# Kernel tuning notes

Hardware: AMD Instinct MI355X
Metric: run time of the kernel (lower is better)

Reference implementation:

```python
import jax, jax.numpy as jnp
import numpy as np

K_NN = 16  # number of nearest neighbors (module init arg k)


def setup_inputs() -> dict:
    key = jax.random.key(0)
    k1, k2 = jax.random.split(key)
    xyz = jax.random.normal(k1, (8, 16384, 3), dtype=jnp.float32)
    centers = jax.random.normal(k2, (8, 1024, 3), dtype=jnp.float32)
    return {"xyz": xyz, "centers": centers}


def reference(xyz, centers):
    # avoiding the (B, N, K, 3) broadcast intermediate of the original while
    # computing the same torch.norm(xyz - centers, dim=-1) math.
    x_sq = jnp.sum(xyz * xyz, axis=-1)          # (B, N)
    c_sq = jnp.sum(centers * centers, axis=-1)  # (B, K)
    cross = jnp.einsum('bnd,bkd->bnk', xyz, centers)  # (B, N, K)
    d2 = x_sq[:, :, None] + c_sq[None if False else slice(None), None, :] - 2.0 * cross
    dist = jnp.sqrt(jnp.maximum(d2, 0.0))       # (B, N, K)
    # torch.topk(dist, k, dim=1, largest=False, sorted=True):
    # smallest-k over the N (points) axis, per center.
    neg = -jnp.transpose(dist, (0, 2, 1))       # (B, K, N)
    _, idx = jax.lax.top_k(neg, K_NN)           # (B, K, k), ascending distance
    return jnp.transpose(idx, (0, 2, 1))        # (B, k, K) to match torch dim=1 topk
```

## Files before the change

kernel.cpp:

```cpp
#include <hip/hip_runtime.h>
#include <stdint.h>

#define BB    8
#define NN    16384
#define KK    1024
#define KNN   16
#define QTR   (NN / 4)
#define QGRP  (QTR / 4)
#define PGRP  256
#define HCAP  96

typedef unsigned long long u64;
typedef float f32x2 __attribute__((ext_vector_type(2)));

__device__ __forceinline__ f32x2 pk_fma(f32x2 a, f32x2 b, f32x2 c) {
    f32x2 d;
    asm("v_pk_fma_f32 %0, %1, %2, %3" : "=v"(d) : "v"(a), "v"(b), "v"(c));
    return d;
}
__device__ __forceinline__ f32x2 pk_mul(f32x2 a, f32x2 b) {
    f32x2 d;
    asm("v_pk_mul_f32 %0, %1, %2" : "=v"(d) : "v"(a), "v"(b));
    return d;
}
__device__ __forceinline__ f32x2 pk_add(f32x2 a, f32x2 b) {
    f32x2 d;
    asm("v_pk_add_f32 %0, %1, %2" : "=v"(d) : "v"(a), "v"(b));
    return d;
}

__device__ __forceinline__ u64 shfl_xor_u64(u64 v, int mask) {
    int lo = (int)(uint32_t)v;
    int hi = (int)(uint32_t)(v >> 32);
    lo = __shfl_xor(lo, mask, 64);
    hi = __shfl_xor(hi, mask, 64);
    return ((u64)(uint32_t)hi << 32) | (u64)(uint32_t)lo;
}

__device__ __forceinline__ u64 shfl_u64(u64 v, int src) {
    int lo = __shfl((int)(uint32_t)v, src, 64);
    int hi = __shfl((int)(uint32_t)(v >> 32), src, 64);
    return ((u64)(uint32_t)hi << 32) | (u64)(uint32_t)lo;
}

__device__ __forceinline__ u64 wave_min_u64(u64 v) {
#pragma unroll
    for (int off = 32; off > 0; off >>= 1) {
        u64 o = shfl_xor_u64(v, off);
        v = o < v ? o : v;
    }
    return v;
}

__device__ __forceinline__ void sort64_kv(u64& key, uint32_t& pay, int lane) {
#pragma unroll
    for (int k = 2; k <= 64; k <<= 1) {
#pragma unroll
        for (int j = k >> 1; j > 0; j >>= 1) {
            u64 okey = shfl_xor_u64(key, j);
            uint32_t opay = (uint32_t)__shfl_xor((int)pay, j, 64);
            bool tmin = ((lane & j) == 0) == ((lane & k) == 0);
            bool osm = okey < key;
            bool take = tmin ? osm : !osm;
            if (take) { key = okey; pay = opay; }
        }
    }
}

__device__ __forceinline__ void sort64_k(u64& key, int lane) {
#pragma unroll
    for (int k = 2; k <= 64; k <<= 1) {
#pragma unroll
        for (int j = k >> 1; j > 0; j >>= 1) {
            u64 okey = shfl_xor_u64(key, j);
            bool tmin = ((lane & j) == 0) == ((lane & k) == 0);
            bool osm = okey < key;
            bool take = tmin ? osm : !osm;
            if (take) key = okey;
        }
    }
}

__device__ __forceinline__ float point_d2(const float* xb, int i,
                                          float c0, float c1, float c2, float csq) {
#pragma clang fp contract(off)
    float x0 = xb[i * 3 + 0];
    float x1 = xb[i * 3 + 1];
    float x2 = xb[i * 3 + 2];
    float xsq = (x0 * x0 + x1 * x1) + x2 * x2;
    float cross = __fmaf_rn(x2, c2, __fmaf_rn(x1, c1, x0 * c0));
    float d2 = (xsq + csq) - 2.0f * cross;
    return d2 < 0.0f ? 0.0f : d2;
}

__device__ __attribute__((noinline)) int fallback_scan(const float* xb,
                                                       float c0, float c1, float c2,
                                                       float csq, int lane) {
    u64 list[KNN];
#pragma unroll
    for (int j = 0; j < KNN; ++j) list[j] = ~0ull;
    for (int i = lane; i < NN; i += 64) {
        float d2 = point_d2(xb, i, c0, c1, c2, csq);
        float dist = __fsqrt_rn(d2);
        u64 key = ((u64)__float_as_uint(dist) << 32) | (u64)(uint32_t)i;
        if (key < list[KNN - 1]) {
#pragma unroll
            for (int j = 0; j < KNN; ++j) {
                bool lt = key < list[j];
                u64 lo = lt ? key : list[j];
                u64 hi = lt ? list[j] : key;
                list[j] = lo;
                key = hi;
            }
        }
    }
    int res = 0;
    for (int it = 0; it < KNN; ++it) {
        u64 best = wave_min_u64(list[0]);
        if (it == lane) res = (int)(uint32_t)best;
        if (list[0] == best) {
#pragma unroll
            for (int j = 0; j < KNN - 1; ++j) list[j] = list[j + 1];
            list[KNN - 1] = ~0ull;
        }
    }
    return res;
}

__device__ __forceinline__ float sixteenth_smallest(float m, int lane) {
    uint32_t u = __float_as_uint(m);
    uint32_t s = (u & 0x80000000u) ? ~u : (u | 0x80000000u);
    u64 v = ((u64)s << 32) | (unsigned)lane;
#pragma unroll
    for (int k = 2; k <= 64; k <<= 1) {
#pragma unroll
        for (int j = k >> 1; j > 0; j >>= 1) {
            u64 o = shfl_xor_u64(v, j);
            bool up = (lane & k) == 0;
            bool takeMin = ((lane & j) == 0) == up;
            u64 mn = v < o ? v : o;
            u64 mx = v < o ? o : v;
            v = takeMin ? mn : mx;
        }
    }
    uint32_t sb = (uint32_t)__shfl((int)(uint32_t)(v >> 32), 15, 64);
    uint32_t ub = (sb & 0x80000000u) ? (sb ^ 0x80000000u) : ~sb;
    return __uint_as_float(ub);
}

__device__ __forceinline__ void load_pairs_aos(const float4* x4, int g,
                                               f32x2& xl, f32x2& xh,
                                               f32x2& yl, f32x2& yh,
                                               f32x2& zl, f32x2& zh,
                                               f32x2& sl, f32x2& sh) {
    float4 f0 = x4[g * 3 + 0];
    float4 f1 = x4[g * 3 + 1];
    float4 f2 = x4[g * 3 + 2];
    xl = f32x2{f0.x, f0.w};  yl = f32x2{f0.y, f1.x};  zl = f32x2{f0.z, f1.y};
    xh = f32x2{f1.z, f2.y};  yh = f32x2{f1.w, f2.z};  zh = f32x2{f2.x, f2.w};
    sl = pk_add(pk_add(pk_mul(xl, xl), pk_mul(yl, yl)), pk_mul(zl, zl));
    sh = pk_add(pk_add(pk_mul(xh, xh), pk_mul(yh, yh)), pk_mul(zh, zh));
}

__global__ __launch_bounds__(256, 8) void knn_kernel(const float* __restrict__ xyz,
                                                     const float* __restrict__ centers,
                                                     int* __restrict__ out) {
#pragma clang fp contract(off)
    const int q = (int)(threadIdx.x >> 6);
    const int lane = (int)(threadIdx.x & 63);
    const int cbase = (int)blockIdx.x * 4;
    const int b = cbase >> 10;

    __shared__ float    s_min[4][256];
    __shared__ float    s_T[4];
    __shared__ int      s_cnt[4][4];
    __shared__ uint32_t s_idx[4][4][HCAP];

    f32x2 nx[4], ny[4], nz[4];
#pragma unroll
    for (int c = 0; c < 4; ++c) {
        float a0 = -2.0f * centers[(cbase + c) * 3 + 0];
        float a1 = -2.0f * centers[(cbase + c) * 3 + 1];
        float a2 = -2.0f * centers[(cbase + c) * 3 + 2];
        nx[c] = f32x2{a0, a0};
        ny[c] = f32x2{a1, a1};
        nz[c] = f32x2{a2, a2};
    }

    const float* xb = xyz + (size_t)b * NN * 3;
    const float4* x4 = (const float4*)xb;
    const int gbase = q * QGRP;

    float m[4];
#pragma unroll
    for (int c = 0; c < 4; ++c) m[c] = __builtin_inff();
#pragma unroll 2
    for (int s = 0; s < PGRP / 64; ++s) {
        int g = gbase + s * 64 + lane;
        f32x2 xl, xh, yl, yh, zl, zh, sl, sh;
        load_pairs_aos(x4, g, xl, xh, yl, yh, zl, zh, sl, sh);
#pragma unroll
        for (int c = 0; c < 4; ++c) {
            f32x2 dl = pk_fma(xl, nx[c], pk_fma(yl, ny[c], pk_fma(zl, nz[c], sl)));
            f32x2 dh = pk_fma(xh, nx[c], pk_fma(yh, ny[c], pk_fma(zh, nz[c], sh)));
            m[c] = fminf(m[c], fminf(fminf(dl.x, dl.y), fminf(dh.x, dh.y)));
        }
    }
#pragma unroll
    for (int c = 0; c < 4; ++c) s_min[c][threadIdx.x] = m[c];
    if (threadIdx.x < 16) s_cnt[threadIdx.x >> 2][threadIdx.x & 3] = 0;
    __syncthreads();
    {
        float v = fminf(fminf(s_min[q][lane], s_min[q][64 + lane]),
                        fminf(s_min[q][128 + lane], s_min[q][192 + lane]));
        float t = sixteenth_smallest(v, lane);
        if (lane == 0) s_T[q] = t;
    }
    __syncthreads();
    float U[4];
#pragma unroll
    for (int c = 0; c < 4; ++c) {
        float T = s_T[c];
        U[c] = T + fabsf(T) * 1e-5f + 5e-4f;
    }

#pragma unroll 2
    for (int s = 0; s < QGRP / 64; ++s) {
        int g = gbase + s * 64 + lane;
        f32x2 xl, xh, yl, yh, zl, zh, sl, sh;
        load_pairs_aos(x4, g, xl, xh, yl, yh, zl, zh, sl, sh);
        int ibase = g * 4;
#pragma unroll
        for (int c = 0; c < 4; ++c) {
            f32x2 dl = pk_fma(xl, nx[c], pk_fma(yl, ny[c], pk_fma(zl, nz[c], sl)));
            f32x2 dh = pk_fma(xh, nx[c], pk_fma(yh, ny[c], pk_fma(zh, nz[c], sh)));
            if (dl.x <= U[c]) {
                int pos = atomicAdd(&s_cnt[c][q], 1);
                if (pos < HCAP) s_idx[c][q][pos] = (uint32_t)(ibase + 0);
            }
            if (dl.y <= U[c]) {
                int pos = atomicAdd(&s_cnt[c][q], 1);
                if (pos < HCAP) s_idx[c][q][pos] = (uint32_t)(ibase + 1);
            }
            if (dh.x <= U[c]) {
                int pos = atomicAdd(&s_cnt[c][q], 1);
                if (pos < HCAP) s_idx[c][q][pos] = (uint32_t)(ibase + 2);
            }
            if (dh.y <= U[c]) {
                int pos = atomicAdd(&s_cnt[c][q], 1);
                if (pos < HCAP) s_idx[c][q][pos] = (uint32_t)(ibase + 3);
            }
        }
    }
    __syncthreads();

    const int cc = cbase + q;
    const float c0 = centers[cc * 3 + 0];
    const float c1 = centers[cc * 3 + 1];
    const float c2 = centers[cc * 3 + 2];
    const float csq = (c0 * c0 + c1 * c1) + c2 * c2;
    const int k0 = s_cnt[q][0], k1 = s_cnt[q][1], k2 = s_cnt[q][2], k3 = s_cnt[q][3];
    const int p1o = k0, p2o = k0 + k1, p3o = k0 + k1 + k2;
    const int total = p3o + k3;
    const bool ok = (k0 <= HCAP) & (k1 <= HCAP) & (k2 <= HCAP) & (k3 <= HCAP) &
                    (total <= 4 * 64);

    uint32_t res;
    if (ok) {
        u64 l0 = ~0ull, l1 = ~0ull, l2 = ~0ull, l3 = ~0ull;
        for (int j = lane; j < total; j += 64) {
            int qq, off;
            if (j < p1o)      { qq = 0; off = j; }
            else if (j < p2o) { qq = 1; off = j - p1o; }
            else if (j < p3o) { qq = 2; off = j - p2o; }
            else              { qq = 3; off = j - p3o; }
            int idx = (int)s_idx[q][qq][off];
            float d2 = point_d2(xb, idx, c0, c1, c2, csq);
            u64 key = ((u64)__float_as_uint(__fsqrt_rn(d2)) << 32) | (u64)(uint32_t)idx;
            bool t;
            t = key < l0; { u64 lo = t ? key : l0, hi = t ? l0 : key; l0 = lo; key = hi; }
            t = key < l1; { u64 lo = t ? key : l1, hi = t ? l1 : key; l1 = lo; key = hi; }
            t = key < l2; { u64 lo = t ? key : l2, hi = t ? l2 : key; l2 = lo; key = hi; }
            t = key < l3; { u64 lo = t ? key : l3, hi = t ? l3 : key; l3 = lo; key = hi; }
        }
        u64 key = l0;
        uint32_t pay = (uint32_t)lane;
        sort64_kv(key, pay, lane);
        int pos = lane >> 2, elem = lane & 3;
        int sid = __shfl((int)pay, pos, 64);
        u64 g0 = shfl_u64(l0, sid);
        u64 g1 = shfl_u64(l1, sid);
        u64 g2 = shfl_u64(l2, sid);
        u64 g3 = shfl_u64(l3, sid);
        u64 gk = (elem == 0) ? g0 : (elem == 1) ? g1 : (elem == 2) ? g2 : g3;
        sort64_k(gk, lane);
        res = (uint32_t)gk;
    } else {
        res = (uint32_t)fallback_scan(xb, c0, c1, c2, csq, lane);
    }

    if (lane < KNN) {
        out[((size_t)b * KNN + lane) * KK + (cc & 1023)] = (int)res;
    }
}

extern "C" void kernel_launch(void* const* d_in, const int* in_sizes, int n_in,
                              void* d_out, int out_size, void* d_ws, size_t ws_size,
                              hipStream_t stream) {
    const float* xyz = (const float*)d_in[0];
    const float* centers = (const float*)d_in[1];
    int* out = (int*)d_out;
    (void)d_ws; (void)ws_size;

    const int nblocks = BB * KK / 4;
    hipLaunchKernelGGL(knn_kernel, dim3(nblocks), dim3(256), 0, stream,
                       xyz, centers, out);
}
```

Baseline: 98.89 us.

## Replace sample-threshold plus full rescan with group-min pruning and targeted rescan

The kernel no longer builds a threshold from a sampled subset of points and then rescans all points against it. A single full pass now records the minimum partial distance of each 16-point group in shared memory. The 16th smallest of those group minima gives a threshold, and only groups under the threshold are re-evaluated to collect candidates. This removes one full distance pass and most of the per-point atomics, at the cost of a larger shared-memory footprint (s_gmin is 16 KB per block), extra shuffles, and a second, irregular gather pass.

After: 95.79 us. -3.1%, faster.

```diff
diff --git a/kernel.cpp b/kernel.cpp
--- a/kernel.cpp
+++ b/kernel.cpp
@@ -7,8 +7,9 @@
 #define KNN   16
 #define QTR   (NN / 4)
 #define QGRP  (QTR / 4)
-#define PGRP  256
-#define HCAP  96
+#define NG16  (NN / 16)
+#define GCAP  48
+#define SCAP  192
 
 typedef unsigned long long u64;
 typedef float f32x2 __attribute__((ext_vector_type(2)));
@@ -171,10 +172,11 @@
     const int cbase = (int)blockIdx.x * 4;
     const int b = cbase >> 10;
 
-    __shared__ float    s_min[4][256];
-    __shared__ float    s_T[4];
-    __shared__ int      s_cnt[4][4];
-    __shared__ uint32_t s_idx[4][4][HCAP];
+    __shared__ float    s_gmin[4][NG16];
+    __shared__ uint32_t s_glist[4][GCAP];
+    __shared__ uint32_t s_idx[4][SCAP];
+    __shared__ int      s_gcnt[4];
+    __shared__ int      s_cnt[4];
 
     f32x2 nx[4], ny[4], nz[4];
 #pragma unroll
@@ -191,97 +193,98 @@
     const float4* x4 = (const float4*)xb;
     const int gbase = q * QGRP;
 
-    float m[4];
-#pragma unroll
-    for (int c = 0; c < 4; ++c) m[c] = __builtin_inff();
-#pragma unroll 2
-    for (int s = 0; s < PGRP / 64; ++s) {
-        int g = gbase + s * 64 + lane;
-        f32x2 xl, xh, yl, yh, zl, zh, sl, sh;
-        load_pairs_aos(x4, g, xl, xh, yl, yh, zl, zh, sl, sh);
-#pragma unroll
-        for (int c = 0; c < 4; ++c) {
-            f32x2 dl = pk_fma(xl, nx[c], pk_fma(yl, ny[c], pk_fma(zl, nz[c], sl)));
-            f32x2 dh = pk_fma(xh, nx[c], pk_fma(yh, ny[c], pk_fma(zh, nz[c], sh)));
-            m[c] = fminf(m[c], fminf(fminf(dl.x, dl.y), fminf(dh.x, dh.y)));
-        }
-    }
-#pragma unroll
-    for (int c = 0; c < 4; ++c) s_min[c][threadIdx.x] = m[c];
-    if (threadIdx.x < 16) s_cnt[threadIdx.x >> 2][threadIdx.x & 3] = 0;
-    __syncthreads();
-    {
-        float v = fminf(fminf(s_min[q][lane], s_min[q][64 + lane]),
-                        fminf(s_min[q][128 + lane], s_min[q][192 + lane]));
-        float t = sixteenth_smallest(v, lane);
-        if (lane == 0) s_T[q] = t;
-    }
-    __syncthreads();
-    float U[4];
-#pragma unroll
-    for (int c = 0; c < 4; ++c) {
-        float T = s_T[c];
-        U[c] = T + fabsf(T) * 1e-5f + 5e-4f;
-    }
+    if (threadIdx.x < 4) { s_gcnt[threadIdx.x] = 0; s_cnt[threadIdx.x] = 0; }
 
 #pragma unroll 2
     for (int s = 0; s < QGRP / 64; ++s) {
         int g = gbase + s * 64 + lane;
         f32x2 xl, xh, yl, yh, zl, zh, sl, sh;
         load_pairs_aos(x4, g, xl, xh, yl, yh, zl, zh, sl, sh);
-        int ibase = g * 4;
+        float gm[4];
 #pragma unroll
         for (int c = 0; c < 4; ++c) {
             f32x2 dl = pk_fma(xl, nx[c], pk_fma(yl, ny[c], pk_fma(zl, nz[c], sl)));
             f32x2 dh = pk_fma(xh, nx[c], pk_fma(yh, ny[c], pk_fma(zh, nz[c], sh)));
-            if (dl.x <= U[c]) {
-                int pos = atomicAdd(&s_cnt[c][q], 1);
-                if (pos < HCAP) s_idx[c][q][pos] = (uint32_t)(ibase + 0);
-            }
-            if (dl.y <= U[c]) {
-                int pos = atomicAdd(&s_cnt[c][q], 1);
-                if (pos < HCAP) s_idx[c][q][pos] = (uint32_t)(ibase + 1);
-            }
-            if (dh.x <= U[c]) {
-                int pos = atomicAdd(&s_cnt[c][q], 1);
-                if (pos < HCAP) s_idx[c][q][pos] = (uint32_t)(ibase + 2);
-            }
-            if (dh.y <= U[c]) {
-                int pos = atomicAdd(&s_cnt[c][q], 1);
-                if (pos < HCAP) s_idx[c][q][pos] = (uint32_t)(ibase + 3);
-            }
+            float v = fminf(fminf(dl.x, dl.y), fminf(dh.x, dh.y));
+            v = fminf(v, __shfl_xor(v, 1, 64));
+            v = fminf(v, __shfl_xor(v, 2, 64));
+            gm[c] = v;
+        }
+        if ((lane & 3) == 0) {
+            int gi = g >> 2;
+#pragma unroll
+            for (int c = 0; c < 4; ++c) s_gmin[c][gi] = gm[c];
         }
     }
     __syncthreads();
+
+    float lm = __builtin_inff();
+#pragma unroll
+    for (int it = 0; it < NG16 / 64; ++it)
+        lm = fminf(lm, s_gmin[q][it * 64 + lane]);
+    float t = sixteenth_smallest(lm, lane);
+    const float Uq = t + fabsf(t) * 1e-5f + 5e-4f;
+
+#pragma unroll
+    for (int it = 0; it < NG16 / 64; ++it) {
+        int gi = it * 64 + lane;
+        if (s_gmin[q][gi] <= Uq) {
+            int pos = atomicAdd(&s_gcnt[q], 1);
+            if (pos < GCAP) s_glist[q][pos] = (uint32_t)gi;
+        }
+    }
+    __syncthreads();
+
+    const int ng = s_gcnt[q];
+    bool ok = (ng <= GCAP);
+
+    if (ok) {
+        for (int j = lane; j < ng * 4; j += 64) {
+            int lg = (int)s_glist[q][j >> 2] * 4 + (j & 3);
+            f32x2 xl, xh, yl, yh, zl, zh, sl, sh;
+            load_pairs_aos(x4, lg, xl, xh, yl, yh, zl, zh, sl, sh);
+            f32x2 dl = pk_fma(xl, nx[q], pk_fma(yl, ny[q], pk_fma(zl, nz[q], sl)));
+            f32x2 dh = pk_fma(xh, nx[q], pk_fma(yh, ny[q], pk_fma(zh, nz[q], sh)));
+            int ibase = lg * 4;
+            if (dl.x <= Uq) {
+                int pos = atomicAdd(&s_cnt[q], 1);
+                if (pos < SCAP) s_idx[q][pos] = (uint32_t)(ibase + 0);
+            }
+            if (dl.y <= Uq) {
+                int pos = atomicAdd(&s_cnt[q], 1);
+                if (pos < SCAP) s_idx[q][pos] = (uint32_t)(ibase + 1);
+            }
+            if (dh.x <= Uq) {
+                int pos = atomicAdd(&s_cnt[q], 1);
+                if (pos < SCAP) s_idx[q][pos] = (uint32_t)(ibase + 2);
+            }
+            if (dh.y <= Uq) {
+                int pos = atomicAdd(&s_cnt[q], 1);
+                if (pos < SCAP) s_idx[q][pos] = (uint32_t)(ibase + 3);
+            }
+        }
+    }
 
     const int cc = cbase + q;
     const float c0 = centers[cc * 3 + 0];
     const float c1 = centers[cc * 3 + 1];
     const float c2 = centers[cc * 3 + 2];
     const float csq = (c0 * c0 + c1 * c1) + c2 * c2;
-    const int k0 = s_cnt[q][0], k1 = s_cnt[q][1], k2 = s_cnt[q][2], k3 = s_cnt[q][3];
-    const int p1o = k0, p2o = k0 + k1, p3o = k0 + k1 + k2;
-    const int total = p3o + k3;
-    const bool ok = (k0 <= HCAP) & (k1 <= HCAP) & (k2 <= HCAP) & (k3 <= HCAP) &
-                    (total <= 4 * 64);
+    const int total = s_cnt[q];
+    ok = ok && (total <= SCAP);
 
     uint32_t res;
     if (ok) {
         u64 l0 = ~0ull, l1 = ~0ull, l2 = ~0ull, l3 = ~0ull;
         for (int j = lane; j < total; j += 64) {
-            int qq, off;
-            if (j < p1o)      { qq = 0; off = j; }
-            else if (j < p2o) { qq = 1; off = j - p1o; }
-            else if (j < p3o) { qq = 2; off = j - p2o; }
-            else              { qq = 3; off = j - p3o; }
-            int idx = (int)s_idx[q][qq][off];
+            int idx = (int)s_idx[q][j];
             float d2 = point_d2(xb, idx, c0, c1, c2, csq);
             u64 key = ((u64)__float_as_uint(__fsqrt_rn(d2)) << 32) | (u64)(uint32_t)idx;
-            bool t;
-            t = key < l0; { u64 lo = t ? key : l0, hi = t ? l0 : key; l0 = lo; key = hi; }
-            t = key < l1; { u64 lo = t ? key : l1, hi = t ? l1 : key; l1 = lo; key = hi; }
-            t = key < l2; { u64 lo = t ? key : l2, hi = t ? l2 : key; l2 = lo; key = hi; }
-            t = key < l3; { u64 lo = t ? key : l3, hi = t ? l3 : key; l3 = lo; key = hi; }
+            bool tt;
+            tt = key < l0; { u64 lo = tt ? key : l0, hi = tt ? l0 : key; l0 = lo; key = hi; }
+            tt = key < l1; { u64 lo = tt ? key : l1, hi = tt ? l1 : key; l1 = lo; key = hi; }
+            tt = key < l2; { u64 lo = tt ? key : l2, hi = tt ? l2 : key; l2 = lo; key = hi; }
+            tt = key < l3; { u64 lo = tt ? key : l3, hi = tt ? l3 : key; l3 = lo; key = hi; }
         }
         u64 key = l0;
         uint32_t pay = (uint32_t)lane;
```
